# Optimization experiments

Hardware: AMD Instinct MI355X
Metric: run time of the kernel (lower is better)

Reference implementation:

```python
import jax, jax.numpy as jnp
import numpy as np
from jax import lax

# 8-bit symmetric quantization: clip bound = 2**(prec-1) - 1
CLIP = 127.0
EPS = 1e-6  # epsilon in scale denominator to avoid div-by-zero (mirrors QuantOps bound epsilon)


def setup_inputs() -> dict:
    key = jax.random.key(0)
    k1, k2 = jax.random.split(key)
    B, CIN, COUT = 8192, 4096, 8192
    act = jax.random.normal(k1, (B, CIN), dtype=jnp.float32)
    w = jax.random.normal(k2, (CIN, COUT), dtype=jnp.float32)
    return {"act": act, "w": w}


def reference(act, w):
    # --- activation quantization: per-input-channel symmetric scale, shape (1, Cin) ---
    act_bound = jnp.max(jnp.abs(act), axis=0, keepdims=True) + EPS     # (1, Cin)
    act_scale = CLIP / act_bound                                        # (1, Cin)
    act_q = jnp.clip(jnp.round(act * act_scale), -CLIP, CLIP)           # int values in fp32

    # fold inverse activation scale into weight rows: w_scaled_rows = (1/act_scale) * w
    w_scaled = w * (1.0 / act_scale).reshape(-1, 1)                     # (Cin, Cout)

    # --- weight quantization: per-output-channel symmetric scale, shape (1, Cout) ---
    w_bound = jnp.max(jnp.abs(w_scaled), axis=0, keepdims=True) + EPS   # (1, Cout)
    w_scale = CLIP / w_bound                                            # (1, Cout)
    w_q = jnp.clip(jnp.round(w_scaled * w_scale), -CLIP, CLIP)

    out_i32 = lax.dot_general(
        act_q.astype(jnp.int8),
        w_q.astype(jnp.int8),
        dimension_numbers=(((1,), (0,)), ((), ())),
        preferred_element_type=jnp.int32,
    )
    out = out_i32.astype(jnp.float32)

    # inline dequant by per-output-channel weight scale (act scale already folded into w)
    return (out * (1.0 / w_scale)).astype(jnp.float32)
```

## Files before the change

kernel.cpp:

```cpp
#include <hip/hip_runtime.h>
#include <hip/hip_bf16.h>
#include <stdint.h>

#define BDIM 8192
#define CIN  4096
#define COUT 8192
#define EPSQ 1e-6f

typedef int v4i __attribute__((ext_vector_type(4)));

#define GLD16_TO_LDS(gp, lp)                                                   \
    __builtin_amdgcn_global_load_lds(                                          \
        (const __attribute__((address_space(1))) void*)(gp),                   \
        (__attribute__((address_space(3))) void*)(lp), 16, 0, 0)

__device__ __forceinline__ int q8i(float x) {
    float r = rintf(x);
    r = fminf(127.0f, fmaxf(-127.0f, r));
    return (int)r;
}

__global__ void act_absmax_kernel(const float* __restrict__ act,
                                  int* __restrict__ amax_bits) {
    int c4 = (blockIdx.x << 8) + threadIdx.x;
    int r0 = blockIdx.y << 5;
    const float4* p = (const float4*)act + (size_t)r0 * (CIN / 4) + c4;
    float mx = 0.f, my = 0.f, mz = 0.f, mw = 0.f;
#pragma unroll 4
    for (int r = 0; r < 32; ++r) {
        float4 v = p[(size_t)r * (CIN / 4)];
        mx = fmaxf(mx, fabsf(v.x));
        my = fmaxf(my, fabsf(v.y));
        mz = fmaxf(mz, fabsf(v.z));
        mw = fmaxf(mw, fabsf(v.w));
    }
    int c = c4 << 2;
    atomicMax(amax_bits + c + 0, __float_as_int(mx));
    atomicMax(amax_bits + c + 1, __float_as_int(my));
    atomicMax(amax_bits + c + 2, __float_as_int(mz));
    atomicMax(amax_bits + c + 3, __float_as_int(mw));
}

__global__ void act_quant_kernel(const float4* __restrict__ act4,
                                 const int4* __restrict__ amax_bits4,
                                 float* __restrict__ inv_as,
                                 int* __restrict__ actq_packed) {
    int flat4 = blockIdx.x * 256 + threadIdx.x;
    int c4 = flat4 & ((CIN / 4) - 1);
    float4 v = act4[flat4];
    int4 mb = amax_bits4[c4];
    float sx = 127.0f / (__int_as_float(mb.x) + EPSQ);
    float sy = 127.0f / (__int_as_float(mb.y) + EPSQ);
    float sz = 127.0f / (__int_as_float(mb.z) + EPSQ);
    float sw = 127.0f / (__int_as_float(mb.w) + EPSQ);
    int q0 = q8i(v.x * sx), q1 = q8i(v.y * sy), q2 = q8i(v.z * sz), q3 = q8i(v.w * sw);
    int packed = (q0 & 0xff) | ((q1 & 0xff) << 8) | ((q2 & 0xff) << 16) | ((q3 & 0xff) << 24);
    actq_packed[flat4] = packed;
    if (flat4 < CIN / 4) {
        int c = c4 << 2;
        inv_as[c + 0] = 1.0f / sx;
        inv_as[c + 1] = 1.0f / sy;
        inv_as[c + 2] = 1.0f / sz;
        inv_as[c + 3] = 1.0f / sw;
    }
}

__global__ void w_absmax_kernel(const float* __restrict__ w,
                                const float* __restrict__ inv_as,
                                int* __restrict__ wmax_bits) {
    int c4 = (blockIdx.x << 8) + threadIdx.x;
    int k0 = blockIdx.y << 4;
    const float4* p = (const float4*)w + (size_t)k0 * (COUT / 4) + c4;
    float mx = 0.f, my = 0.f, mz = 0.f, mw = 0.f;
#pragma unroll 4
    for (int r = 0; r < 16; ++r) {
        float ia = inv_as[k0 + r];
        float4 v = p[(size_t)r * (COUT / 4)];
        mx = fmaxf(mx, fabsf(v.x * ia));
        my = fmaxf(my, fabsf(v.y * ia));
        mz = fmaxf(mz, fabsf(v.z * ia));
        mw = fmaxf(mw, fabsf(v.w * ia));
    }
    int c = c4 << 2;
    atomicMax(wmax_bits + c + 0, __float_as_int(mx));
    atomicMax(wmax_bits + c + 1, __float_as_int(my));
    atomicMax(wmax_bits + c + 2, __float_as_int(mz));
    atomicMax(wmax_bits + c + 3, __float_as_int(mw));
}

__global__ void w_quant_t_kernel(const float* __restrict__ w,
                                 const float* __restrict__ inv_as,
                                 const int* __restrict__ wmax_bits,
                                 signed char* __restrict__ wqT) {
    __shared__ float lf[32 * 132];
    int t = threadIdx.x;
    int k0 = blockIdx.x << 7;
    int j0 = blockIdx.y << 5;
    const float4* w4 = (const float4*)w;
#pragma unroll
    for (int it = 0; it < 4; ++it) {
        int idx = it * 256 + t;
        int kk = idx >> 3;
        int j4 = idx & 7;
        float4 v = w4[(size_t)(k0 + kk) * (COUT / 4) + (j0 >> 2) + j4];
        lf[(j4 * 4 + 0) * 132 + kk] = v.x;
        lf[(j4 * 4 + 1) * 132 + kk] = v.y;
        lf[(j4 * 4 + 2) * 132 + kk] = v.z;
        lf[(j4 * 4 + 3) * 132 + kk] = v.w;
    }
    __syncthreads();
#pragma unroll
    for (int it = 0; it < 4; ++it) {
        int kq = t & 31;
        int jl = (t >> 5) + (it << 3);
        int j = j0 + jl;
        float wscale = 127.0f / (__int_as_float(wmax_bits[j]) + EPSQ);
        float4 f = *(const float4*)(lf + jl * 132 + (kq << 2));
        int kb = k0 + (kq << 2);
        float w0 = f.x * inv_as[kb + 0];
        float w1 = f.y * inv_as[kb + 1];
        float w2 = f.z * inv_as[kb + 2];
        float w3 = f.w * inv_as[kb + 3];
        int q0 = q8i(w0 * wscale), q1 = q8i(w1 * wscale);
        int q2 = q8i(w2 * wscale), q3 = q8i(w3 * wscale);
        int packed = (q0 & 0xff) | ((q1 & 0xff) << 8) |
                     ((q2 & 0xff) << 16) | ((q3 & 0xff) << 24);
        *(int*)(wqT + (size_t)j * CIN + kb) = packed;
    }
}

__global__ __launch_bounds__(512, 2) void gemm_i8_kernel(
    const signed char* __restrict__ Aq,
    const signed char* __restrict__ Bq,
    const int* __restrict__ wmax_bits,
    float* __restrict__ out) {
    __shared__ __align__(16) signed char lds[131072];
    signed char* As = lds;
    signed char* Bs = lds + 65536;

    const int tid = threadIdx.x;
    const int wave = tid >> 6;
    const int lane = tid & 63;
    const int g = lane >> 4;
    const int l16 = lane & 15;

    const int bid = blockIdx.x;
    const int xcd = bid & 7, idx = bid >> 3;
    const int rg = xcd >> 2, cg = xcd & 3;
    const int bm = (((rg << 4) + (idx >> 3)) << 8);
    const int bn = (((cg << 3) + (idx & 7)) << 8);

    const int wm128 = (wave >> 2) << 7;
    const int wn64 = (wave & 3) << 6;

    const int m = tid & 255;
    const int gq = tid >> 8;
    const signed char* aP = Aq + ((size_t)(bm + m) << 12) + (gq << 4);
    const signed char* bP = Bq + ((size_t)(bn + m) << 12) + (gq << 4);
    const int ldsOff = tid << 4;

    const int offA = ((g << 8) + wm128 + l16) << 4;
    const int offB = ((g << 8) + wn64 + l16) << 4;

    v4i acc[8][4] = {};
    v4i fA0[4], fA1[4], fB[4];

#define STAGE_A(t_)                                                            \
    do {                                                                       \
        signed char* d_ = As + (((t_) & 3) << 14);                             \
        const int kb_ = (t_) << 6;                                             \
        GLD16_TO_LDS(aP + kb_,      d_ + ldsOff);                              \
        GLD16_TO_LDS(aP + kb_ + 32, d_ + 8192 + ldsOff);                       \
    } while (0)
#define STAGE_B(t_)                                                            \
    do {                                                                       \
        signed char* d_ = Bs + (((t_) & 3) << 14);                             \
        const int kb_ = (t_) << 6;                                             \
        GLD16_TO_LDS(bP + kb_,      d_ + ldsOff);                              \
        GLD16_TO_LDS(bP + kb_ + 32, d_ + 8192 + ldsOff);                       \
    } while (0)
#define READ_FA0(s_)                                                           \
    do {                                                                       \
        const signed char* Ab_ = As + (((s_) & 3) << 14);                      \
        _Pragma("unroll")                                                      \
        for (int t = 0; t < 4; ++t)                                            \
            fA0[t] = *(const v4i*)(Ab_ + offA + (t << 8));                     \
    } while (0)
#define READ_FA1(s_)                                                           \
    do {                                                                       \
        const signed char* Ab_ = As + (((s_) & 3) << 14);                      \
        _Pragma("unroll")                                                      \
        for (int t = 0; t < 4; ++t)                                            \
            fA1[t] = *(const v4i*)(Ab_ + offA + ((t + 4) << 8));               \
    } while (0)
#define READ_FB(s_)                                                            \
    do {                                                                       \
        const signed char* Bb_ = Bs + (((s_) & 3) << 14);                      \
        _Pragma("unroll")                                                      \
        for (int t = 0; t < 4; ++t)                                            \
            fB[t] = *(const v4i*)(Bb_ + offB + (t << 8));                      \
    } while (0)
#define MFMA_LO                                                                \
    do {                                                                       \
        __builtin_amdgcn_s_setprio(1);                                         \
        _Pragma("unroll")                                                      \
        for (int tm = 0; tm < 4; ++tm)                                         \
            _Pragma("unroll")                                                  \
            for (int tn = 0; tn < 4; ++tn)                                     \
                acc[tm][tn] = __builtin_amdgcn_mfma_i32_16x16x64_i8(           \
                    fA0[tm], fB[tn], acc[tm][tn], 0, 0, 0);                    \
        __builtin_amdgcn_s_setprio(0);                                         \
    } while (0)
#define MFMA_HI                                                                \
    do {                                                                       \
        __builtin_amdgcn_s_setprio(1);                                         \
        _Pragma("unroll")                                                      \
        for (int tm = 0; tm < 4; ++tm)                                         \
            _Pragma("unroll")                                                  \
            for (int tn = 0; tn < 4; ++tn)                                     \
                acc[tm + 4][tn] = __builtin_amdgcn_mfma_i32_16x16x64_i8(       \
                    fA1[tm], fB[tn], acc[tm + 4][tn], 0, 0, 0);                \
        __builtin_amdgcn_s_setprio(0);                                         \
    } while (0)

    STAGE_A(0); STAGE_B(0);
    STAGE_A(1); STAGE_B(1);
    STAGE_A(2); STAGE_B(2);
    asm volatile("s_waitcnt vmcnt(8)" ::: "memory");
    __builtin_amdgcn_s_barrier();
    READ_FA0(0);
    READ_FB(0);

#pragma unroll 1
    for (int s = 0; s < 61; ++s) {
        __builtin_amdgcn_s_barrier();
        __builtin_amdgcn_sched_barrier(0);
        STAGE_A(s + 3);
        MFMA_LO;
        READ_FA1(s);
        asm volatile("s_waitcnt vmcnt(6)" ::: "memory");
        __builtin_amdgcn_sched_barrier(0);
        __builtin_amdgcn_s_barrier();
        __builtin_amdgcn_sched_barrier(0);
        STAGE_B(s + 3);
        MFMA_HI;
        READ_FA0(s + 1);
        READ_FB(s + 1);
        __builtin_amdgcn_sched_barrier(0);
    }

    asm volatile("s_waitcnt vmcnt(0)" ::: "memory");
    __builtin_amdgcn_s_barrier();
    __builtin_amdgcn_sched_barrier(0);
    MFMA_LO;
    READ_FA1(61);
    MFMA_HI;
    READ_FA0(62); READ_FB(62);
    MFMA_LO;
    READ_FA1(62);
    MFMA_HI;
    READ_FA0(63); READ_FB(63);
    MFMA_LO;
    READ_FA1(63);
    MFMA_HI;

#undef STAGE_A
#undef STAGE_B
#undef READ_FA0
#undef READ_FA1
#undef READ_FB
#undef MFMA_LO
#undef MFMA_HI

#pragma unroll
    for (int tn = 0; tn < 4; ++tn) {
        int col = bn + wn64 + (tn << 4) + l16;
        float wscale = 127.0f / (__int_as_float(wmax_bits[col]) + EPSQ);
        float invws = 1.0f / wscale;
#pragma unroll
        for (int tm = 0; tm < 8; ++tm) {
            int row0 = bm + wm128 + (tm << 4) + (g << 2);
#pragma unroll
            for (int r = 0; r < 4; ++r)
                out[((size_t)(row0 + r) << 13) + col] = (float)acc[tm][tn][r] * invws;
        }
    }
}

extern "C" void kernel_launch(void* const* d_in, const int* in_sizes, int n_in,
                              void* d_out, int out_size, void* d_ws, size_t ws_size,
                              hipStream_t stream) {
    const float* act = (const float*)d_in[0];
    const float* w   = (const float*)d_in[1];
    float* out = (float*)d_out;
    char* ws = (char*)d_ws;

    int*   amax_bits = (int*)ws;
    float* inv_as    = (float*)(ws + 16384);
    int*   wmax_bits = (int*)(ws + 32768);
    signed char* actq = (signed char*)(ws + 65536);
    signed char* wqT  = (signed char*)(ws + 65536 + (size_t)BDIM * CIN);

    act_absmax_kernel<<<dim3(4, 256), 256, 0, stream>>>(act, amax_bits);
    act_quant_kernel<<<(BDIM * CIN / 4) / 256, 256, 0, stream>>>(
        (const float4*)act, (const int4*)amax_bits, inv_as, (int*)actq);
    w_absmax_kernel<<<dim3(8, 256), 256, 0, stream>>>(w, inv_as, wmax_bits);
    w_quant_t_kernel<<<dim3(32, 256), 256, 0, stream>>>(w, inv_as, wmax_bits, wqT);
    gemm_i8_kernel<<<COUT / 256 * (BDIM / 256), 512, 0, stream>>>(
        actq, wqT, wmax_bits, out);
}
```

Baseline: 875.1 us.

## Shrink GEMM tile to 128x128 with triple-buffered LDS and coarsen absmax reductions

The int8 GEMM goes from 256x256 tiles with 512 threads and a 4-stage split A/B pipeline to 128x128 tiles with 256 threads, a 3-buffer rotating LDS ring and a single combined stage/read/MFMA step per k-iteration. The smaller LDS footprint lets three blocks share a CU, trading less operand reuse per block for more occupancy and a simpler schedule. The absmax kernels each process four times more rows per block, which cuts the number of atomicMax operations. The smaller tiles increase global and L2 traffic for A and B.

```diff
diff --git a/kernel.cpp b/kernel.cpp
--- a/kernel.cpp
+++ b/kernel.cpp
@@ -23,11 +23,11 @@
 __global__ void act_absmax_kernel(const float* __restrict__ act,
                                   int* __restrict__ amax_bits) {
     int c4 = (blockIdx.x << 8) + threadIdx.x;
-    int r0 = blockIdx.y << 5;
+    int r0 = blockIdx.y << 7;
     const float4* p = (const float4*)act + (size_t)r0 * (CIN / 4) + c4;
     float mx = 0.f, my = 0.f, mz = 0.f, mw = 0.f;
 #pragma unroll 4
-    for (int r = 0; r < 32; ++r) {
+    for (int r = 0; r < 128; ++r) {
         float4 v = p[(size_t)r * (CIN / 4)];
         mx = fmaxf(mx, fabsf(v.x));
         my = fmaxf(my, fabsf(v.y));
@@ -69,11 +69,11 @@
                                 const float* __restrict__ inv_as,
                                 int* __restrict__ wmax_bits) {
     int c4 = (blockIdx.x << 8) + threadIdx.x;
-    int k0 = blockIdx.y << 4;
+    int k0 = blockIdx.y << 6;
     const float4* p = (const float4*)w + (size_t)k0 * (COUT / 4) + c4;
     float mx = 0.f, my = 0.f, mz = 0.f, mw = 0.f;
 #pragma unroll 4
-    for (int r = 0; r < 16; ++r) {
+    for (int r = 0; r < 64; ++r) {
         float ia = inv_as[k0 + r];
         float4 v = p[(size_t)r * (COUT / 4)];
         mx = fmaxf(mx, fabsf(v.x * ia));
@@ -129,14 +129,14 @@
     }
 }
 
-__global__ __launch_bounds__(512, 2) void gemm_i8_kernel(
+__global__ __launch_bounds__(256, 3) void gemm_i8_kernel(
     const signed char* __restrict__ Aq,
     const signed char* __restrict__ Bq,
     const int* __restrict__ wmax_bits,
     float* __restrict__ out) {
-    __shared__ __align__(16) signed char lds[131072];
+    __shared__ __align__(16) signed char lds[49152];
     signed char* As = lds;
-    signed char* Bs = lds + 65536;
+    signed char* Bs = lds + 24576;
 
     const int tid = threadIdx.x;
     const int wave = tid >> 6;
@@ -147,60 +147,42 @@
     const int bid = blockIdx.x;
     const int xcd = bid & 7, idx = bid >> 3;
     const int rg = xcd >> 2, cg = xcd & 3;
-    const int bm = (((rg << 4) + (idx >> 3)) << 8);
-    const int bn = (((cg << 3) + (idx & 7)) << 8);
-
-    const int wm128 = (wave >> 2) << 7;
-    const int wn64 = (wave & 3) << 6;
-
-    const int m = tid & 255;
-    const int gq = tid >> 8;
-    const signed char* aP = Aq + ((size_t)(bm + m) << 12) + (gq << 4);
-    const signed char* bP = Bq + ((size_t)(bn + m) << 12) + (gq << 4);
+    const int bm = ((rg << 5) + (idx >> 4)) << 7;
+    const int bn = ((cg << 4) + (idx & 15)) << 7;
+
+    const int wm64 = (wave >> 1) << 6;
+    const int wn64 = (wave & 1) << 6;
+
+    const int m = tid & 127;
+    const int k16 = (tid >> 7) << 4;
+    const signed char* aP = Aq + ((size_t)(bm + m) << 12) + k16;
+    const signed char* bP = Bq + ((size_t)(bn + m) << 12) + k16;
     const int ldsOff = tid << 4;
 
-    const int offA = ((g << 8) + wm128 + l16) << 4;
-    const int offB = ((g << 8) + wn64 + l16) << 4;
-
-    v4i acc[8][4] = {};
-    v4i fA0[4], fA1[4], fB[4];
-
-#define STAGE_A(t_)                                                            \
+    const int offA = ((g << 7) + wm64 + l16) << 4;
+    const int offB = ((g << 7) + wn64 + l16) << 4;
+
+    v4i acc[4][4] = {};
+    v4i fA[4], fB[4];
+
+#define STAGE_STEP(s_, wa_)                                                    \
     do {                                                                       \
-        signed char* d_ = As + (((t_) & 3) << 14);                             \
-        const int kb_ = (t_) << 6;                                             \
-        GLD16_TO_LDS(aP + kb_,      d_ + ldsOff);                              \
-        GLD16_TO_LDS(aP + kb_ + 32, d_ + 8192 + ldsOff);                       \
+        const int kb_ = (s_) << 6;                                             \
+        GLD16_TO_LDS(aP + kb_,      As + (wa_) + ldsOff);                      \
+        GLD16_TO_LDS(aP + kb_ + 32, As + (wa_) + 4096 + ldsOff);               \
+        GLD16_TO_LDS(bP + kb_,      Bs + (wa_) + ldsOff);                      \
+        GLD16_TO_LDS(bP + kb_ + 32, Bs + (wa_) + 4096 + ldsOff);               \
     } while (0)
-#define STAGE_B(t_)                                                            \
+#define READ_FRAGS(ra_)                                                        \
     do {                                                                       \
-        signed char* d_ = Bs + (((t_) & 3) << 14);                             \
-        const int kb_ = (t_) << 6;                                             \
-        GLD16_TO_LDS(bP + kb_,      d_ + ldsOff);                              \
-        GLD16_TO_LDS(bP + kb_ + 32, d_ + 8192 + ldsOff);                       \
-    } while (0)
-#define READ_FA0(s_)                                                           \
-    do {                                                                       \
-        const signed char* Ab_ = As + (((s_) & 3) << 14);                      \
         _Pragma("unroll")                                                      \
         for (int t = 0; t < 4; ++t)                                            \
-            fA0[t] = *(const v4i*)(Ab_ + offA + (t << 8));                     \
-    } while (0)
-#define READ_FA1(s_)                                                           \
-    do {                                                                       \
-        const signed char* Ab_ = As + (((s_) & 3) << 14);                      \
+            fA[t] = *(const v4i*)(As + (ra_) + offA + (t << 8));               \
         _Pragma("unroll")                                                      \
         for (int t = 0; t < 4; ++t)                                            \
-            fA1[t] = *(const v4i*)(Ab_ + offA + ((t + 4) << 8));               \
+            fB[t] = *(const v4i*)(Bs + (ra_) + offB + (t << 8));               \
     } while (0)
-#define READ_FB(s_)                                                            \
-    do {                                                                       \
-        const signed char* Bb_ = Bs + (((s_) & 3) << 14);                      \
-        _Pragma("unroll")                                                      \
-        for (int t = 0; t < 4; ++t)                                            \
-            fB[t] = *(const v4i*)(Bb_ + offB + (t << 8));                      \
-    } while (0)
-#define MFMA_LO                                                                \
+#define MFMA_ALL                                                               \
     do {                                                                       \
         __builtin_amdgcn_s_setprio(1);                                         \
         _Pragma("unroll")                                                      \
@@ -208,69 +190,43 @@
             _Pragma("unroll")                                                  \
             for (int tn = 0; tn < 4; ++tn)                                     \
                 acc[tm][tn] = __builtin_amdgcn_mfma_i32_16x16x64_i8(           \
-                    fA0[tm], fB[tn], acc[tm][tn], 0, 0, 0);                    \
+                    fA[tm], fB[tn], acc[tm][tn], 0, 0, 0);                     \
         __builtin_amdgcn_s_setprio(0);                                         \
     } while (0)
-#define MFMA_HI                                                                \
-    do {                                                                       \
-        __builtin_amdgcn_s_setprio(1);                                         \
-        _Pragma("unroll")                                                      \
-        for (int tm = 0; tm < 4; ++tm)                                         \
-            _Pragma("unroll")                                                  \
-            for (int tn = 0; tn < 4; ++tn)                                     \
-                acc[tm + 4][tn] = __builtin_amdgcn_mfma_i32_16x16x64_i8(       \
-                    fA1[tm], fB[tn], acc[tm + 4][tn], 0, 0, 0);                \
-        __builtin_amdgcn_s_setprio(0);                                         \
-    } while (0)
-
-    STAGE_A(0); STAGE_B(0);
-    STAGE_A(1); STAGE_B(1);
-    STAGE_A(2); STAGE_B(2);
-    asm volatile("s_waitcnt vmcnt(8)" ::: "memory");
-    __builtin_amdgcn_s_barrier();
-    READ_FA0(0);
-    READ_FB(0);
+
+    int ra = 0, na = 8192, wa = 16384;
+
+    STAGE_STEP(0, 0);
+    STAGE_STEP(1, 8192);
+    asm volatile("s_waitcnt vmcnt(4)" ::: "memory");
 
 #pragma unroll 1
-    for (int s = 0; s < 61; ++s) {
+    for (int s = 0; s < 62; ++s) {
         __builtin_amdgcn_s_barrier();
         __builtin_amdgcn_sched_barrier(0);
-        STAGE_A(s + 3);
-        MFMA_LO;
-        READ_FA1(s);
-        asm volatile("s_waitcnt vmcnt(6)" ::: "memory");
+        STAGE_STEP(s + 2, wa);
         __builtin_amdgcn_sched_barrier(0);
-        __builtin_amdgcn_s_barrier();
+        READ_FRAGS(ra);
+        MFMA_ALL;
+        asm volatile("s_waitcnt vmcnt(4)" ::: "memory");
         __builtin_amdgcn_sched_barrier(0);
-        STAGE_B(s + 3);
-        MFMA_HI;
-        READ_FA0(s + 1);
-        READ_FB(s + 1);
-        __builtin_amdgcn_sched_barrier(0);
-    }
-
-    asm volatile("s_waitcnt vmcnt(0)" ::: "memory");
+        int t_ = ra; ra = na; na = wa; wa = t_;
+    }
+
     __builtin_amdgcn_s_barrier();
     __builtin_amdgcn_sched_barrier(0);
-    MFMA_LO;
-    READ_FA1(61);
-    MFMA_HI;
-    READ_FA0(62); READ_FB(62);
-    MFMA_LO;
-    READ_FA1(62);
-    MFMA_HI;
-    READ_FA0(63); READ_FB(63);
-    MFMA_LO;
-    READ_FA1(63);
-    MFMA_HI;
-
-#undef STAGE_A
-#undef STAGE_B
-#undef READ_FA0
-#undef READ_FA1
-#undef READ_FB
-#undef MFMA_LO
-#undef MFMA_HI
+    READ_FRAGS(ra);
+    MFMA_ALL;
+    asm volatile("s_waitcnt vmcnt(0)" ::: "memory");
+    __builtin_amdgcn_sched_barrier(0);
+    __builtin_amdgcn_s_barrier();
+    __builtin_amdgcn_sched_barrier(0);
+    READ_FRAGS(na);
+    MFMA_ALL;
+
+#undef STAGE_STEP
+#undef READ_FRAGS
+#undef MFMA_ALL
 
 #pragma unroll
     for (int tn = 0; tn < 4; ++tn) {
@@ -278,8 +234,8 @@
         float wscale = 127.0f / (__int_as_float(wmax_bits[col]) + EPSQ);
         float invws = 1.0f / wscale;
 #pragma unroll
-        for (int tm = 0; tm < 8; ++tm) {
-            int row0 = bm + wm128 + (tm << 4) + (g << 2);
+        for (int tm = 0; tm < 4; ++tm) {
+            int row0 = bm + wm64 + (tm << 4) + (g << 2);
 #pragma unroll
             for (int r = 0; r < 4; ++r)
                 out[((size_t)(row0 + r) << 13) + col] = (float)acc[tm][tn][r] * invws;
@@ -301,11 +257,11 @@
     signed char* actq = (signed char*)(ws + 65536);
     signed char* wqT  = (signed char*)(ws + 65536 + (size_t)BDIM * CIN);
 
-    act_absmax_kernel<<<dim3(4, 256), 256, 0, stream>>>(act, amax_bits);
+    act_absmax_kernel<<<dim3(4, 64), 256, 0, stream>>>(act, amax_bits);
     act_quant_kernel<<<(BDIM * CIN / 4) / 256, 256, 0, stream>>>(
         (const float4*)act, (const int4*)amax_bits, inv_as, (int*)actq);
-    w_absmax_kernel<<<dim3(8, 256), 256, 0, stream>>>(w, inv_as, wmax_bits);
+    w_absmax_kernel<<<dim3(8, 64), 256, 0, stream>>>(w, inv_as, wmax_bits);
     w_quant_t_kernel<<<dim3(32, 256), 256, 0, stream>>>(w, inv_as, wmax_bits, wqT);
-    gemm_i8_kernel<<<COUT / 256 * (BDIM / 256), 512, 0, stream>>>(
+    gemm_i8_kernel<<<(COUT / 128) * (BDIM / 128), 256, 0, stream>>>(
         actq, wqT, wmax_bits, out);
 }
```

Measured after the change: 1.038 ms. 1.19x slower.
